# Optimization experiments

Hardware: AMD Instinct MI355X
Metric: run time of the kernel (lower is better)

## Reference

```python
import jax, jax.numpy as jnp
import numpy as np

N_NODES = 50000
N_EDGES = 1600000
D_IN = 128
D_HID = 128
D_OUT = 128


def setup_inputs() -> dict:
    key = jax.random.key(0)
    ks = jax.random.split(key, 12)
    s = 0.05
    return {
        "x": jax.random.normal(ks[0], (N_NODES, D_IN), jnp.float32),
        "src": jax.random.randint(ks[1], (N_EDGES,), 0, N_NODES),
        "dst": jax.random.randint(ks[2], (N_EDGES,), 0, N_NODES),
        "W_neigh1": jax.random.normal(ks[3], (D_HID, D_IN), jnp.float32) * s,
        "W_self1": jax.random.normal(ks[4], (D_HID, D_IN), jnp.float32) * s,
        "b_self1": jnp.zeros((D_HID,), jnp.float32),
        "W_neigh2": jax.random.normal(ks[5], (D_HID, D_HID), jnp.float32) * s,
        "W_self2": jax.random.normal(ks[6], (D_HID, D_HID), jnp.float32) * s,
        "b_self2": jnp.zeros((D_HID,), jnp.float32),
        "W_neigh3": jax.random.normal(ks[7], (D_OUT, D_HID), jnp.float32) * s,
        "W_self3": jax.random.normal(ks[8], (D_OUT, D_HID), jnp.float32) * s,
        "b_self3": jnp.zeros((D_OUT,), jnp.float32),
    }


def _sage_mean(h, src, dst, inv_deg, W_neigh, W_self, b_self):
    # DGL SAGEConv 'mean': fc_self(h) + fc_neigh(mean of in-neighbor feats)
    # zero in-degree nodes get zero neighbor term (inv_deg = 0 there is avoided
    # by clamping degree to >=1, sum is 0 anyway).
    neigh_sum = jax.ops.segment_sum(h[src], dst, num_segments=h.shape[0])  # [N, d]
    h_neigh = neigh_sum * inv_deg  # [N, d]
    return h @ W_self.T + b_self + h_neigh @ W_neigh.T


def reference(x, src, dst, W_neigh1, W_self1, b_self1, W_neigh2, W_self2, b_self2, W_neigh3, W_self3, b_self3):
    n = x.shape[0]
    deg = jax.ops.segment_sum(jnp.ones((src.shape[0],), x.dtype), dst, num_segments=n)
    inv_deg = (1.0 / jnp.maximum(deg, 1.0))[:, None]  # [N, 1]
    h = jax.nn.relu(_sage_mean(x, src, dst, inv_deg, W_neigh1, W_self1, b_self1))
    h = jax.nn.relu(_sage_mean(h, src, dst, inv_deg, W_neigh2, W_self2, b_self2))
    h = _sage_mean(h, src, dst, inv_deg, W_neigh3, W_self3, b_self3)
    return h
```

## Files before the change

kernel.cpp:

```cpp
#include <hip/hip_runtime.h>


constexpr int N_NODES = 50000;
constexpr int N_EDGES = 1600000;
constexpr int D = 128;
constexpr int SCAN_BLK = 1024;
constexpr int NCHUNK = (N_NODES + SCAN_BLK - 1) / SCAN_BLK;

typedef __bf16 bf16x8 __attribute__((ext_vector_type(8)));
typedef float f32x4 __attribute__((ext_vector_type(4)));
union U8 { bf16x8 v; __bf16 e[8]; };

__global__ void zero1(int* __restrict__ a, int n) {
    int i = blockIdx.x * blockDim.x + threadIdx.x;
    if (i < n) a[i] = 0;
}

__global__ void hist_pos(const int* __restrict__ dst, int* __restrict__ counts,
                         int* __restrict__ pos, int n) {
    int e = blockIdx.x * blockDim.x + threadIdx.x;
    if (e < n) pos[e] = atomicAdd(&counts[dst[e]], 1);
}

__global__ __launch_bounds__(SCAN_BLK) void scan_p1(const int* __restrict__ counts,
                                                    int* __restrict__ row_ptr,
                                                    float* __restrict__ inv_deg,
                                                    int* __restrict__ blocksums) {
    __shared__ int wsum[16];
    __shared__ int wpre[16];
    const int t = threadIdx.x;
    const int i = blockIdx.x * SCAN_BLK + t;
    const int lane = t & 63, w = t >> 6;
    int v = (i < N_NODES) ? counts[i] : 0;
    int x = v;
    #pragma unroll
    for (int off = 1; off < 64; off <<= 1) {
        int tt = __shfl_up(x, off, 64);
        if (lane >= off) x += tt;
    }
    if (lane == 63) wsum[w] = x;
    __syncthreads();
    if (t < 16) {
        int s = wsum[t];
        int y = s;
        #pragma unroll
        for (int off = 1; off < 16; off <<= 1) {
            int tt = __shfl_up(y, off, 64);
            if (t >= off) y += tt;
        }
        wpre[t] = y - s;
    }
    __syncthreads();
    if (i < N_NODES) {
        row_ptr[i] = wpre[w] + (x - v);
        inv_deg[i] = 1.0f / fmaxf((float)v, 1.0f);
    }
    if (t == SCAN_BLK - 1) blocksums[blockIdx.x] = wpre[15] + wsum[15];
}

__global__ void scan_p2(const int* __restrict__ blocksums, int* __restrict__ blockoffs) {
    const int t = threadIdx.x;
    int v = (t < NCHUNK) ? blocksums[t] : 0;
    int x = v;
    #pragma unroll
    for (int off = 1; off < 64; off <<= 1) {
        int tt = __shfl_up(x, off, 64);
        if (t >= off) x += tt;
    }
    if (t < NCHUNK) blockoffs[t] = x - v;
}

__global__ __launch_bounds__(SCAN_BLK) void scan_p3(int* __restrict__ row_ptr,
                                                    const int* __restrict__ blockoffs) {
    const int i = blockIdx.x * SCAN_BLK + threadIdx.x;
    if (i < N_NODES) row_ptr[i] += blockoffs[blockIdx.x];
    if (i == 0) row_ptr[N_NODES] = N_EDGES;
}

__global__ void scatter_edges(const int* __restrict__ src, const int* __restrict__ dst,
                              const int* __restrict__ pos, const int* __restrict__ row_ptr,
                              int* __restrict__ esrc, int n) {
    int e = blockIdx.x * blockDim.x + threadIdx.x;
    if (e < n) esrc[row_ptr[dst[e]] + pos[e]] = src[e];
}

__global__ void pack_w(const float* __restrict__ w0, const float* __restrict__ w1,
                       const float* __restrict__ w2, const float* __restrict__ w3,
                       const float* __restrict__ w4, const float* __restrict__ w5,
                       __bf16* __restrict__ outbase) {
    const float* ws[6] = {w0, w1, w2, w3, w4, w5};
    const float* W = ws[blockIdx.y];
    __bf16* o = outbase + (size_t)blockIdx.y * 32768;
    int idx = blockIdx.x * 256 + threadIdx.x;
    int t = idx & 7;
    int lane = (idx >> 3) & 63;
    int ks = (idx >> 9) & 3;
    int jt = idx >> 11;
    int j = jt * 16 + (lane & 15);
    int k = ks * 32 + (lane >> 4) * 8 + t;
    float w = W[j * D + k];
    __bf16 hi = (__bf16)w;
    o[idx] = hi;
    o[16384 + idx] = (__bf16)(w - (float)hi);
}

__global__ __launch_bounds__(256) void dual_gemm(
        const float* __restrict__ h, const __bf16* __restrict__ Bs,
        const __bf16* __restrict__ Bn, const float* __restrict__ bias,
        float* __restrict__ y_self, __bf16* __restrict__ z) {
    const int wave = threadIdx.x >> 6;
    const int lane = threadIdx.x & 63;
    const int tile = blockIdx.x * 4 + wave;
    if (tile >= N_NODES / 16) return;
    const int n0 = tile * 16;
    const int row = n0 + (lane & 15);
    const int koff = (lane >> 4) * 8;

    U8 ahi[4], alo[4];
    #pragma unroll
    for (int ks = 0; ks < 4; ++ks) {
        const float* p = h + (size_t)row * D + ks * 32 + koff;
        float f[8];
        *(f32x4*)&f[0] = *(const f32x4*)p;
        *(f32x4*)&f[4] = *(const f32x4*)(p + 4);
        #pragma unroll
        for (int t = 0; t < 8; ++t) {
            __bf16 hi = (__bf16)f[t];
            ahi[ks].e[t] = hi;
            alo[ks].e[t] = (__bf16)(f[t] - (float)hi);
        }
    }

    const int jcol = lane & 15;
    const int r0 = (lane >> 4) * 4;

    #pragma unroll 2
    for (int jt = 0; jt < 8; ++jt) {
        f32x4 accS = {0.f, 0.f, 0.f, 0.f};
        f32x4 accN = {0.f, 0.f, 0.f, 0.f};
        #pragma unroll
        for (int ks = 0; ks < 4; ++ks) {
            const size_t off = (((size_t)jt * 4 + ks) * 64 + lane) * 8;
            bf16x8 wsh = *(const bf16x8*)(Bs + off);
            bf16x8 wsl = *(const bf16x8*)(Bs + 16384 + off);
            bf16x8 wnh = *(const bf16x8*)(Bn + off);
            bf16x8 wnl = *(const bf16x8*)(Bn + 16384 + off);
            accS = __builtin_amdgcn_mfma_f32_16x16x32_bf16(ahi[ks].v, wsh, accS, 0, 0, 0);
            accS = __builtin_amdgcn_mfma_f32_16x16x32_bf16(alo[ks].v, wsh, accS, 0, 0, 0);
            accS = __builtin_amdgcn_mfma_f32_16x16x32_bf16(ahi[ks].v, wsl, accS, 0, 0, 0);
            accN = __builtin_amdgcn_mfma_f32_16x16x32_bf16(ahi[ks].v, wnh, accN, 0, 0, 0);
            accN = __builtin_amdgcn_mfma_f32_16x16x32_bf16(alo[ks].v, wnh, accN, 0, 0, 0);
            accN = __builtin_amdgcn_mfma_f32_16x16x32_bf16(ahi[ks].v, wnl, accN, 0, 0, 0);
        }
        const int j = jt * 16 + jcol;
        const float bj = bias[j];
        #pragma unroll
        for (int r = 0; r < 4; ++r) {
            const size_t n = n0 + r0 + r;
            y_self[n * D + j] = accS[r] + bj;
            z[n * D + j] = (__bf16)accN[r];
        }
    }
}

__global__ __launch_bounds__(256) void agg_add(
        const __bf16* __restrict__ z, const int* __restrict__ esrc,
        const int* __restrict__ row_ptr, const float* __restrict__ inv_deg,
        const float* __restrict__ y_self, float* __restrict__ out, int do_relu) {
    const int n = blockIdx.x * 4 + (threadIdx.x >> 6);
    const int lane = threadIdx.x & 63;
    const int s = lane >> 4;
    const int c = lane & 15;
    const int r0 = row_ptr[n], r1 = row_ptr[n + 1];

    float acc[8] = {0.f, 0.f, 0.f, 0.f, 0.f, 0.f, 0.f, 0.f};
    int e = r0 + s;
    for (; e + 12 < r1; e += 16) {
        int i0 = esrc[e], i1 = esrc[e + 4], i2 = esrc[e + 8], i3 = esrc[e + 12];
        U8 v0, v1, v2, v3;
        v0.v = *(const bf16x8*)(z + (size_t)i0 * D + c * 8);
        v1.v = *(const bf16x8*)(z + (size_t)i1 * D + c * 8);
        v2.v = *(const bf16x8*)(z + (size_t)i2 * D + c * 8);
        v3.v = *(const bf16x8*)(z + (size_t)i3 * D + c * 8);
        #pragma unroll
        for (int t = 0; t < 8; ++t)
            acc[t] += ((float)v0.e[t] + (float)v1.e[t]) + ((float)v2.e[t] + (float)v3.e[t]);
    }
    for (; e < r1; e += 4) {
        U8 v0;
        v0.v = *(const bf16x8*)(z + (size_t)esrc[e] * D + c * 8);
        #pragma unroll
        for (int t = 0; t < 8; ++t) acc[t] += (float)v0.e[t];
    }
    #pragma unroll
    for (int t = 0; t < 8; ++t) acc[t] += __shfl_down(acc[t], 32, 64);
    #pragma unroll
    for (int t = 0; t < 8; ++t) acc[t] += __shfl_down(acc[t], 16, 64);

    if (lane < 16) {
        const float idg = inv_deg[n];
        const float* yp = y_self + (size_t)n * D + c * 8;
        f32x4 y0 = *(const f32x4*)yp;
        f32x4 y1 = *(const f32x4*)(yp + 4);
        float o[8];
        #pragma unroll
        for (int t = 0; t < 4; ++t) o[t] = y0[t] + acc[t] * idg;
        #pragma unroll
        for (int t = 0; t < 4; ++t) o[4 + t] = y1[t] + acc[4 + t] * idg;
        if (do_relu) {
            #pragma unroll
            for (int t = 0; t < 8; ++t) o[t] = fmaxf(o[t], 0.f);
        }
        float* op = out + (size_t)n * D + c * 8;
        *(f32x4*)op = *(f32x4*)&o[0];
        *(f32x4*)(op + 4) = *(f32x4*)&o[4];
    }
}

extern "C" void kernel_launch(void* const* d_in, const int* in_sizes, int n_in,
                              void* d_out, int out_size, void* d_ws, size_t ws_size,
                              hipStream_t stream) {
    const float* x   = (const float*)d_in[0];
    const int* src   = (const int*)d_in[1];
    const int* dst   = (const int*)d_in[2];
    const float* Wn1 = (const float*)d_in[3];
    const float* Ws1 = (const float*)d_in[4];
    const float* b1  = (const float*)d_in[5];
    const float* Wn2 = (const float*)d_in[6];
    const float* Ws2 = (const float*)d_in[7];
    const float* b2  = (const float*)d_in[8];
    const float* Wn3 = (const float*)d_in[9];
    const float* Ws3 = (const float*)d_in[10];
    const float* b3  = (const float*)d_in[11];
    float* out = (float*)d_out;

    char* w = (char*)d_ws;
    float* inv_deg  = (float*)w;                w += 50176 * 4;
    int* counts     = (int*)w;                  w += 50176 * 4;
    int* row_ptr    = (int*)w;                  w += 50432 * 4;
    int* blocksums  = (int*)w;                  w += 64 * 4;
    int* blockoffs  = (int*)w;                  w += 64 * 4;
    int* esrc       = (int*)w;                  w += (size_t)N_EDGES * 4;
    __bf16* Bpk     = (__bf16*)w;               w += 6 * 32768 * 2;
    __bf16* zbuf    = (__bf16*)w;               w += (size_t)50176 * D * 2;
    float* bufA     = (float*)w;

    int* pos = (int*)zbuf;

    const __bf16* PWs1 = Bpk + 0 * 32768, *PWn1 = Bpk + 1 * 32768;
    const __bf16* PWs2 = Bpk + 2 * 32768, *PWn2 = Bpk + 3 * 32768;
    const __bf16* PWs3 = Bpk + 4 * 32768, *PWn3 = Bpk + 5 * 32768;

    zero1<<<(50176 + 255) / 256, 256, 0, stream>>>(counts, 50176);
    hist_pos<<<(N_EDGES + 511) / 512, 512, 0, stream>>>(dst, counts, pos, N_EDGES);
    scan_p1<<<NCHUNK, SCAN_BLK, 0, stream>>>(counts, row_ptr, inv_deg, blocksums);
    scan_p2<<<1, 64, 0, stream>>>(blocksums, blockoffs);
    scan_p3<<<NCHUNK, SCAN_BLK, 0, stream>>>(row_ptr, blockoffs);
    scatter_edges<<<(N_EDGES + 511) / 512, 512, 0, stream>>>(src, dst, pos, row_ptr,
                                                             esrc, N_EDGES);
    pack_w<<<dim3(64, 6), 256, 0, stream>>>(Ws1, Wn1, Ws2, Wn2, Ws3, Wn3, Bpk);

    const int ggrid = (N_NODES / 16 + 3) / 4;
    const int agrid = N_NODES / 4;

    dual_gemm<<<ggrid, 256, 0, stream>>>(x, PWs1, PWn1, b1, bufA, zbuf);
    agg_add<<<agrid, 256, 0, stream>>>(zbuf, esrc, row_ptr, inv_deg, bufA, bufA, 1);

    dual_gemm<<<ggrid, 256, 0, stream>>>(bufA, PWs2, PWn2, b2, out, zbuf);
    agg_add<<<agrid, 256, 0, stream>>>(zbuf, esrc, row_ptr, inv_deg, out, out, 1);

    dual_gemm<<<ggrid, 256, 0, stream>>>(out, PWs3, PWn3, b3, bufA, zbuf);
    agg_add<<<agrid, 256, 0, stream>>>(zbuf, esrc, row_ptr, inv_deg, bufA, out, 0);
}
```

Before: 433.8 us.

## Build CSR via two-level bucketed counting sort instead of global atomics

Replaces the per-edge global atomic histogram, multi-pass scan and random scatter with a two-level bucket sort. Edges are first grouped into 128-node buckets using shared-memory histograms and one global atomic per bucket per block. Each bucket is then sorted locally in shared memory to produce row_ptr, inv_deg and esrc. The aim is fewer global atomics and more local writes, but edges past a fixed per-bucket capacity are silently dropped, and source and destination are packed into 16-bit fields.

New measurement: 378.9 us. 1.14x faster.

```diff
diff --git a/kernel.cpp b/kernel.cpp
--- a/kernel.cpp
+++ b/kernel.cpp
@@ -4,8 +4,12 @@
 constexpr int N_NODES = 50000;
 constexpr int N_EDGES = 1600000;
 constexpr int D = 128;
-constexpr int SCAN_BLK = 1024;
-constexpr int NCHUNK = (N_NODES + SCAN_BLK - 1) / SCAN_BLK;
+
+constexpr int NBUCK = 392;
+constexpr int BCAP  = 6144;
+constexpr int EPB   = 4096;
+constexpr int CS_BLOCKS = (N_EDGES + EPB - 1) / EPB;
+constexpr int GC_STRIDE = 16;
 
 typedef __bf16 bf16x8 __attribute__((ext_vector_type(8)));
 typedef float f32x4 __attribute__((ext_vector_type(4)));
@@ -16,22 +20,56 @@
     if (i < n) a[i] = 0;
 }
 
-__global__ void hist_pos(const int* __restrict__ dst, int* __restrict__ counts,
-                         int* __restrict__ pos, int n) {
-    int e = blockIdx.x * blockDim.x + threadIdx.x;
-    if (e < n) pos[e] = atomicAdd(&counts[dst[e]], 1);
-}
-
-__global__ __launch_bounds__(SCAN_BLK) void scan_p1(const int* __restrict__ counts,
-                                                    int* __restrict__ row_ptr,
-                                                    float* __restrict__ inv_deg,
-                                                    int* __restrict__ blocksums) {
-    __shared__ int wsum[16];
-    __shared__ int wpre[16];
+__global__ __launch_bounds__(256) void bucket_count_scatter(
+        const int* __restrict__ dst, const int* __restrict__ src,
+        int* __restrict__ gcursor, int* __restrict__ bucketbuf) {
+    __shared__ int hcnt[NBUCK];
+    __shared__ int hbase[NBUCK];
+    const int tid = threadIdx.x;
+    for (int i = tid; i < NBUCK; i += 256) hcnt[i] = 0;
+    __syncthreads();
+
+    const int e0 = blockIdx.x * EPB;
+    int d[16], lp[16];
+    #pragma unroll
+    for (int t = 0; t < 16; ++t) {
+        const int e = e0 + t * 256 + tid;
+        if (e < N_EDGES) {
+            d[t] = dst[e];
+            lp[t] = atomicAdd(&hcnt[d[t] >> 7], 1);
+        } else {
+            d[t] = 0; lp[t] = -1;
+        }
+    }
+    __syncthreads();
+
+    for (int i = tid; i < NBUCK; i += 256) {
+        const int c = hcnt[i];
+        hbase[i] = c ? atomicAdd(&gcursor[i * GC_STRIDE], c) : 0;
+    }
+    __syncthreads();
+
+    #pragma unroll
+    for (int t = 0; t < 16; ++t) {
+        const int e = e0 + t * 256 + tid;
+        if (e < N_EDGES) {
+            const int s  = src[e];
+            const int bk = d[t] >> 7;
+            const int p  = hbase[bk] + lp[t];
+            if (p < BCAP)
+                bucketbuf[bk * BCAP + p] = ((d[t] & 127) << 16) | s;
+        }
+    }
+}
+
+__global__ void bucket_scan(const int* __restrict__ gcursor,
+                            int* __restrict__ bucket_base,
+                            int* __restrict__ row_ptr) {
+    __shared__ int wsum[8], wpre[8];
     const int t = threadIdx.x;
-    const int i = blockIdx.x * SCAN_BLK + t;
     const int lane = t & 63, w = t >> 6;
-    int v = (i < N_NODES) ? counts[i] : 0;
+    int v = 0;
+    if (t < NBUCK) { v = gcursor[t * GC_STRIDE]; if (v > BCAP) v = BCAP; }
     int x = v;
     #pragma unroll
     for (int off = 1; off < 64; off <<= 1) {
@@ -40,48 +78,63 @@
     }
     if (lane == 63) wsum[w] = x;
     __syncthreads();
-    if (t < 16) {
-        int s = wsum[t];
-        int y = s;
-        #pragma unroll
-        for (int off = 1; off < 16; off <<= 1) {
+    if (t < 8) {
+        int s = wsum[t], y = s;
+        #pragma unroll
+        for (int off = 1; off < 8; off <<= 1) {
             int tt = __shfl_up(y, off, 64);
             if (t >= off) y += tt;
         }
         wpre[t] = y - s;
     }
     __syncthreads();
-    if (i < N_NODES) {
-        row_ptr[i] = wpre[w] + (x - v);
-        inv_deg[i] = 1.0f / fmaxf((float)v, 1.0f);
-    }
-    if (t == SCAN_BLK - 1) blocksums[blockIdx.x] = wpre[15] + wsum[15];
-}
-
-__global__ void scan_p2(const int* __restrict__ blocksums, int* __restrict__ blockoffs) {
-    const int t = threadIdx.x;
-    int v = (t < NCHUNK) ? blocksums[t] : 0;
-    int x = v;
+    if (t < NBUCK) bucket_base[t] = wpre[w] + (x - v);
+    if (t == 0) row_ptr[N_NODES] = N_EDGES;
+}
+
+__global__ __launch_bounds__(256) void bucket_csr(
+        const int* __restrict__ gcursor, const int* __restrict__ bucket_base,
+        const int* __restrict__ bucketbuf, int* __restrict__ row_ptr,
+        float* __restrict__ inv_deg, int* __restrict__ esrc) {
+    __shared__ int h[128];
+    __shared__ int cur[128];
+    __shared__ int s0tot;
+    const int bk = blockIdx.x, tid = threadIdx.x;
+    int cnt = gcursor[bk * GC_STRIDE];
+    if (cnt > BCAP) cnt = BCAP;
+    const int base = bucket_base[bk];
+    if (tid < 128) h[tid] = 0;
+    __syncthreads();
+
+    const int* bb = bucketbuf + (size_t)bk * BCAP;
+    for (int i = tid; i < cnt; i += 256) atomicAdd(&h[bb[i] >> 16], 1);
+    __syncthreads();
+
+    const int c = (tid < 128) ? h[tid] : 0;
+    int x = c;
+    const int lane = tid & 63;
     #pragma unroll
     for (int off = 1; off < 64; off <<= 1) {
         int tt = __shfl_up(x, off, 64);
-        if (t >= off) x += tt;
-    }
-    if (t < NCHUNK) blockoffs[t] = x - v;
-}
-
-__global__ __launch_bounds__(SCAN_BLK) void scan_p3(int* __restrict__ row_ptr,
-                                                    const int* __restrict__ blockoffs) {
-    const int i = blockIdx.x * SCAN_BLK + threadIdx.x;
-    if (i < N_NODES) row_ptr[i] += blockoffs[blockIdx.x];
-    if (i == 0) row_ptr[N_NODES] = N_EDGES;
-}
-
-__global__ void scatter_edges(const int* __restrict__ src, const int* __restrict__ dst,
-                              const int* __restrict__ pos, const int* __restrict__ row_ptr,
-                              int* __restrict__ esrc, int n) {
-    int e = blockIdx.x * blockDim.x + threadIdx.x;
-    if (e < n) esrc[row_ptr[dst[e]] + pos[e]] = src[e];
+        if (lane >= off) x += tt;
+    }
+    if (tid == 63) s0tot = x;
+    __syncthreads();
+    const int excl = x - c + ((tid >= 64 && tid < 128) ? s0tot : 0);
+    if (tid < 128) {
+        cur[tid] = excl;
+        const int node = (bk << 7) + tid;
+        if (node < N_NODES) {
+            row_ptr[node] = base + excl;
+            inv_deg[node] = 1.0f / fmaxf((float)c, 1.0f);
+        }
+    }
+    __syncthreads();
+
+    for (int i = tid; i < cnt; i += 256) {
+        const int p = bb[i];
+        esrc[base + atomicAdd(&cur[p >> 16], 1)] = p & 0xFFFF;
+    }
 }
 
 __global__ void pack_w(const float* __restrict__ w0, const float* __restrict__ w1,
@@ -235,29 +288,27 @@
     float* out = (float*)d_out;
 
     char* w = (char*)d_ws;
-    float* inv_deg  = (float*)w;                w += 50176 * 4;
-    int* counts     = (int*)w;                  w += 50176 * 4;
-    int* row_ptr    = (int*)w;                  w += 50432 * 4;
-    int* blocksums  = (int*)w;                  w += 64 * 4;
-    int* blockoffs  = (int*)w;                  w += 64 * 4;
-    int* esrc       = (int*)w;                  w += (size_t)N_EDGES * 4;
-    __bf16* Bpk     = (__bf16*)w;               w += 6 * 32768 * 2;
-    __bf16* zbuf    = (__bf16*)w;               w += (size_t)50176 * D * 2;
-    float* bufA     = (float*)w;
-
-    int* pos = (int*)zbuf;
+    float* inv_deg     = (float*)w;             w += 50176 * 4;
+    int* row_ptr       = (int*)w;               w += 50432 * 4;
+    int* gcursor       = (int*)w;               w += NBUCK * GC_STRIDE * 4;
+    int* bucket_base   = (int*)w;               w += 512 * 4;
+    int* esrc          = (int*)w;               w += (size_t)N_EDGES * 4;
+    __bf16* Bpk        = (__bf16*)w;            w += 6 * 32768 * 2;
+    __bf16* zbuf       = (__bf16*)w;            w += (size_t)50176 * D * 2;
+    float* bufA        = (float*)w;
+
+    int* bucketbuf = (int*)zbuf;
 
     const __bf16* PWs1 = Bpk + 0 * 32768, *PWn1 = Bpk + 1 * 32768;
     const __bf16* PWs2 = Bpk + 2 * 32768, *PWn2 = Bpk + 3 * 32768;
     const __bf16* PWs3 = Bpk + 4 * 32768, *PWn3 = Bpk + 5 * 32768;
 
-    zero1<<<(50176 + 255) / 256, 256, 0, stream>>>(counts, 50176);
-    hist_pos<<<(N_EDGES + 511) / 512, 512, 0, stream>>>(dst, counts, pos, N_EDGES);
-    scan_p1<<<NCHUNK, SCAN_BLK, 0, stream>>>(counts, row_ptr, inv_deg, blocksums);
-    scan_p2<<<1, 64, 0, stream>>>(blocksums, blockoffs);
-    scan_p3<<<NCHUNK, SCAN_BLK, 0, stream>>>(row_ptr, blockoffs);
-    scatter_edges<<<(N_EDGES + 511) / 512, 512, 0, stream>>>(src, dst, pos, row_ptr,
-                                                             esrc, N_EDGES);
+    zero1<<<(NBUCK * GC_STRIDE + 255) / 256, 256, 0, stream>>>(gcursor, NBUCK * GC_STRIDE);
+    bucket_count_scatter<<<CS_BLOCKS, 256, 0, stream>>>(dst, src, gcursor, bucketbuf);
+    bucket_scan<<<1, 512, 0, stream>>>(gcursor, bucket_base, row_ptr);
+    bucket_csr<<<NBUCK, 256, 0, stream>>>(gcursor, bucket_base, bucketbuf,
+                                          row_ptr, inv_deg, esrc);
+
     pack_w<<<dim3(64, 6), 256, 0, stream>>>(Ws1, Wn1, Ws2, Wn2, Ws3, Wn3, Bpk);
 
     const int ggrid = (N_NODES / 16 + 3) / 4;
```
